# Optimization experiments

Hardware: AMD Instinct MI355X
Metric: run time of the kernel (lower is better)

## Reference

```python
import jax, jax.numpy as jnp
import numpy as np


def setup_inputs() -> dict:
    key = jax.random.key(0)
    k1, k2, k3, k4, k5 = jax.random.split(key, 5)
    n_nodes, input_dim, hidden1 = 100000, 512, 128
    z_dim = hidden1 // 2
    n_edges = 1000000
    X = jax.random.normal(k1, (n_nodes, input_dim), dtype=jnp.float32)
    W = jax.random.normal(k2, (input_dim, hidden1), dtype=jnp.float32) * 0.05
    W2 = jax.random.normal(k3, (hidden1, z_dim), dtype=jnp.float32) * 0.05
    train_edges = jax.random.randint(k4, (n_edges, 2), 0, n_nodes, dtype=jnp.int64)
    train_false_edges = jax.random.randint(k5, (n_edges, 2), 0, n_nodes, dtype=jnp.int64)
    return {"X": X, "W": W, "W2": W2,
            "train_edges": train_edges, "train_false_edges": train_false_edges}


def _decode(z, edges):
    # fused gather -> elementwise mult -> row sum over all edges at once
    # z: [N, d], edges: [E, 2] -> [E, 1]
    return jnp.sum(z[edges[:, 0]] * z[edges[:, 1]], axis=-1, keepdims=True)


def reference(X, W, W2, train_edges, train_false_edges):
    # encode: note torch.mm(adj, x) in the original is dead code; output is
    # activation(x @ W), so adj never affects the result.
    h = jax.nn.relu(X @ W)          # [N, hidden1]
    z = h @ W2                      # [N, z_dim] (identity activation)
    z1 = _decode(z, train_edges)        # [E, 1]
    z2 = _decode(z, train_false_edges)  # [E, 1]
    return jax.nn.sigmoid(jnp.concatenate([z1, z2], axis=0))  # [2E, 1]
```

## Files before the change

### kernel.cpp

```cpp
#include <hip/hip_runtime.h>
#include <hip/hip_bf16.h>
#include <hip/hip_fp16.h>
#include <math.h>

#define IN_DIM 512
#define H1     128
#define ZD     64

typedef __attribute__((ext_vector_type(8))) short bf16x8;
typedef __attribute__((ext_vector_type(4))) float f32x4;

__device__ __forceinline__ ushort f32_to_bf16_bits(float x) {
    unsigned b = __float_as_uint(x);
    unsigned r = (b + 0x7FFF + ((b >> 16) & 1)) >> 16;
    return (ushort)r;
}

__global__ void prepack_w(const float* __restrict__ W,
                          ushort* __restrict__ Whi, ushort* __restrict__ Wlo) {
    int t = blockIdx.x * 256 + threadIdx.x;
    int s  = t >> 9;
    int cb = (t >> 6) & 7;
    int l  = t & 63;
    ushort h[8], lo[8];
    #pragma unroll
    for (int j = 0; j < 8; ++j) {
        int k   = s * 32 + ((l >> 4) * 8) + j;
        int col = cb * 16 + (l & 15);
        float x = W[(size_t)k * H1 + col];
        ushort hb = f32_to_bf16_bits(x);
        float  hf = __uint_as_float((unsigned)hb << 16);
        h[j]  = hb;
        lo[j] = f32_to_bf16_bits(x - hf);
    }
    size_t off = ((size_t)t) * 8;
    *(ushort4*)&Whi[off]     = make_ushort4(h[0], h[1], h[2], h[3]);
    *(ushort4*)&Whi[off + 4] = make_ushort4(h[4], h[5], h[6], h[7]);
    *(ushort4*)&Wlo[off]     = make_ushort4(lo[0], lo[1], lo[2], lo[3]);
    *(ushort4*)&Wlo[off + 4] = make_ushort4(lo[4], lo[5], lo[6], lo[7]);
}

__global__ __launch_bounds__(256, 4) void encode_kernel(
    const float* __restrict__ X, const ushort* __restrict__ Whi,
    const ushort* __restrict__ Wlo, const float* __restrict__ W2,
    __half* __restrict__ Z, int N)
{
    __shared__ __align__(16) union {
        ushort st[2][2][4][512];
        float  ht[H1][68];
    } sm;

    const int tid  = threadIdx.x;
    const int lane = tid & 63;
    const int w    = tid >> 6;
    const int wr   = w >> 1;
    const int wc   = w & 1;
    const int row0 = blockIdx.x * 64;

    const int srow = tid >> 2;
    const int kq   = tid & 3;
    const int srb  = srow >> 4;
    const int sla  = (srow & 15) | (kq << 4);
    const bool srow_ok = (row0 + srow) < N;
    const float* xp = X + (size_t)(row0 + srow) * IN_DIM + kq * 8;

    f32x4 acc[2][4];
    #pragma unroll
    for (int i = 0; i < 2; ++i)
        #pragma unroll
        for (int j = 0; j < 4; ++j) acc[i][j] = (f32x4){0.f, 0.f, 0.f, 0.f};

    float4 rgA, rgB;
    rgA = srow_ok ? *(const float4*)(xp + 0) : make_float4(0, 0, 0, 0);
    rgB = srow_ok ? *(const float4*)(xp + 4) : make_float4(0, 0, 0, 0);

    auto stage = [&](int buf) {
        float xv[8] = {rgA.x, rgA.y, rgA.z, rgA.w, rgB.x, rgB.y, rgB.z, rgB.w};
        unsigned hb[8], lb[8];
        #pragma unroll
        for (int j = 0; j < 8; ++j) {
            unsigned b = __float_as_uint(xv[j]);
            unsigned hf = b & 0xFFFF0000u;
            hb[j] = b;
            lb[j] = __float_as_uint(xv[j] - __uint_as_float(hf));
        }
        uint4 hp, lp;
        hp.x = (hb[0] >> 16) | (hb[1] & 0xFFFF0000u);
        hp.y = (hb[2] >> 16) | (hb[3] & 0xFFFF0000u);
        hp.z = (hb[4] >> 16) | (hb[5] & 0xFFFF0000u);
        hp.w = (hb[6] >> 16) | (hb[7] & 0xFFFF0000u);
        lp.x = (lb[0] >> 16) | (lb[1] & 0xFFFF0000u);
        lp.y = (lb[2] >> 16) | (lb[3] & 0xFFFF0000u);
        lp.z = (lb[4] >> 16) | (lb[5] & 0xFFFF0000u);
        lp.w = (lb[6] >> 16) | (lb[7] & 0xFFFF0000u);
        *(uint4*)&sm.st[buf][0][srb][sla * 8] = hp;
        *(uint4*)&sm.st[buf][1][srb][sla * 8] = lp;
    };

    stage(0);
    rgA = srow_ok ? *(const float4*)(xp + 32) : make_float4(0, 0, 0, 0);
    rgB = srow_ok ? *(const float4*)(xp + 36) : make_float4(0, 0, 0, 0);
    __syncthreads();

    for (int s = 0; s < 16; ++s) {
        const int buf = s & 1;
        bf16x8 aH[2], aL[2];
        #pragma unroll
        for (int rb = 0; rb < 2; ++rb) {
            int rbg = wr * 2 + rb;
            aH[rb] = *(const bf16x8*)&sm.st[buf][0][rbg][lane * 8];
            aL[rb] = *(const bf16x8*)&sm.st[buf][1][rbg][lane * 8];
        }
        if (s < 15) stage(buf ^ 1);
        if (s < 14) {
            const float* xp2 = xp + (s + 2) * 32;
            rgA = srow_ok ? *(const float4*)(xp2 + 0) : make_float4(0, 0, 0, 0);
            rgB = srow_ok ? *(const float4*)(xp2 + 4) : make_float4(0, 0, 0, 0);
        }
        #pragma unroll
        for (int cb = 0; cb < 4; ++cb) {
            int cbg = wc * 4 + cb;
            size_t off = ((size_t)(s * 8 + cbg) * 64 + lane) * 8;
            bf16x8 bH = *(const bf16x8*)&Whi[off];
            bf16x8 bL = *(const bf16x8*)&Wlo[off];
            #pragma unroll
            for (int rb = 0; rb < 2; ++rb) {
                acc[rb][cb] = __builtin_amdgcn_mfma_f32_16x16x32_bf16(
                    aH[rb], bH, acc[rb][cb], 0, 0, 0);
                acc[rb][cb] = __builtin_amdgcn_mfma_f32_16x16x32_bf16(
                    aH[rb], bL, acc[rb][cb], 0, 0, 0);
                acc[rb][cb] = __builtin_amdgcn_mfma_f32_16x16x32_bf16(
                    aL[rb], bH, acc[rb][cb], 0, 0, 0);
            }
        }
        __syncthreads();
    }

    #pragma unroll
    for (int rb = 0; rb < 2; ++rb)
        #pragma unroll
        for (int cb = 0; cb < 4; ++cb) {
            int col = wc * 64 + cb * 16 + (lane & 15);
            int rr  = wr * 32 + rb * 16 + (lane >> 4) * 4;
            #pragma unroll
            for (int r = 0; r < 4; ++r)
                sm.ht[col][rr + r] = fmaxf(acc[rb][cb][r], 0.f);
        }
    __syncthreads();

    const int tx = tid & 31;
    const int ty = tid >> 5;

    float zacc[8][2];
    #pragma unroll
    for (int i = 0; i < 8; ++i) { zacc[i][0] = 0.f; zacc[i][1] = 0.f; }

    #pragma unroll 4
    for (int k = 0; k < H1; ++k) {
        float2 b  = *(const float2*)&W2[(size_t)k * ZD + tx * 2];
        float4 h0 = *(const float4*)&sm.ht[k][ty * 8];
        float4 h1 = *(const float4*)&sm.ht[k][ty * 8 + 4];
        float a[8] = {h0.x, h0.y, h0.z, h0.w, h1.x, h1.y, h1.z, h1.w};
        #pragma unroll
        for (int i = 0; i < 8; ++i) {
            zacc[i][0] = fmaf(a[i], b.x, zacc[i][0]);
            zacc[i][1] = fmaf(a[i], b.y, zacc[i][1]);
        }
    }
    #pragma unroll
    for (int i = 0; i < 8; ++i) {
        int gr = row0 + ty * 8 + i;
        if (gr < N)
            *(__half2*)&Z[(size_t)gr * ZD + tx * 2] =
                __floats2half2_rn(zacc[i][0], zacc[i][1]);
    }
}

__global__ __launch_bounds__(256) void decode_kernel(
    const __half* __restrict__ Zh, const int* __restrict__ e1,
    const int* __restrict__ e2, float* __restrict__ out, int E)
{
    const int tid  = threadIdx.x;
    const int lane = tid & 63;
    const int wv   = tid >> 6;
    const int sub  = lane >> 3;
    const int l    = lane & 7;
    const int total = 2 * E;
    const int stride = gridDim.x * 32;

    for (int idx = (blockIdx.x * 4 + wv) * 8 + sub; idx < total; idx += stride) {
        const int* ep = (idx < E) ? (e1 + 2 * (size_t)idx)
                                  : (e2 + 2 * (size_t)(idx - E));
        int2 ab = *(const int2*)ep;
        union { uint4 u; __half2 h[4]; } A, B;
        A.u = *(const uint4*)&Zh[(size_t)ab.x * ZD + l * 8];
        B.u = *(const uint4*)&Zh[(size_t)ab.y * ZD + l * 8];
        float s = 0.f;
        #pragma unroll
        for (int j = 0; j < 4; ++j) {
            float2 fa = __half22float2(A.h[j]);
            float2 fb = __half22float2(B.h[j]);
            s += fa.x * fb.x + fa.y * fb.y;
        }
        s += __shfl_xor(s, 4, 64);
        s += __shfl_xor(s, 2, 64);
        s += __shfl_xor(s, 1, 64);
        if (l == 0) out[idx] = 1.f / (1.f + __expf(-s));
    }
}

extern "C" void kernel_launch(void* const* d_in, const int* in_sizes, int n_in,
                              void* d_out, int out_size, void* d_ws, size_t ws_size,
                              hipStream_t stream) {
    const float* X  = (const float*)d_in[0];
    const float* W  = (const float*)d_in[1];
    const float* W2 = (const float*)d_in[2];
    const int*   e1 = (const int*)d_in[3];
    const int*   e2 = (const int*)d_in[4];
    float* out = (float*)d_out;

    const int N = in_sizes[0] / IN_DIM;
    const int E = in_sizes[3] / 2;

    __half* Zh  = (__half*)d_ws;
    ushort* Whi = (ushort*)((char*)d_ws + 12800000);
    ushort* Wlo = (ushort*)((char*)d_ws + 12800000 + 131072);

    prepack_w<<<32, 256, 0, stream>>>(W, Whi, Wlo);

    const int nblk = (N + 63) / 64;
    encode_kernel<<<nblk, 256, 0, stream>>>(X, Whi, Wlo, W2, Zh, N);

    decode_kernel<<<2048, 256, 0, stream>>>(Zh, e1, e2, out, E);
}
```

Baseline: 398.0 us.

## Bucket edges by node range before decode and shrink encode hidden staging to fp16

Adds a scatter pass that groups all edges into 128 buckets keyed by the source and destination node ranges. A new decode kernel then walks each bucket, so the Z row gathers from one block hit a narrower address range and should reuse cache better. This costs an extra pass that writes and re-reads 16-byte records, and edges beyond a fixed per-bucket capacity are silently dropped, which is only safe for roughly uniform indices. The encode kernel also stores the ReLU hidden tile as fp16 rather than fp32, raises the launch-bounds occupancy target, and remaps the X staging threads, at some cost in precision.

```diff
diff --git a/kernel.cpp b/kernel.cpp
--- a/kernel.cpp
+++ b/kernel.cpp
@@ -6,6 +6,9 @@
 #define IN_DIM 512
 #define H1     128
 #define ZD     64
+
+#define NBKT   128
+#define BCAP   18432
 
 typedef __attribute__((ext_vector_type(8))) short bf16x8;
 typedef __attribute__((ext_vector_type(4))) float f32x4;
@@ -40,14 +43,14 @@
     *(ushort4*)&Wlo[off + 4] = make_ushort4(lo[4], lo[5], lo[6], lo[7]);
 }
 
-__global__ __launch_bounds__(256, 4) void encode_kernel(
+__global__ __launch_bounds__(256, 8) void encode_kernel(
     const float* __restrict__ X, const ushort* __restrict__ Whi,
     const ushort* __restrict__ Wlo, const float* __restrict__ W2,
     __half* __restrict__ Z, int N)
 {
     __shared__ __align__(16) union {
         ushort st[2][2][4][512];
-        float  ht[H1][68];
+        __half ht[H1][72];
     } sm;
 
     const int tid  = threadIdx.x;
@@ -57,10 +60,10 @@
     const int wc   = w & 1;
     const int row0 = blockIdx.x * 64;
 
-    const int srow = tid >> 2;
-    const int kq   = tid & 3;
-    const int srb  = srow >> 4;
-    const int sla  = (srow & 15) | (kq << 4);
+    const int srb  = tid >> 6;
+    const int sla  = tid & 63;
+    const int srow = srb * 16 + (tid & 15);
+    const int kq   = (tid >> 4) & 3;
     const bool srow_ok = (row0 + srow) < N;
     const float* xp = X + (size_t)(row0 + srow) * IN_DIM + kq * 8;
 
@@ -142,9 +145,10 @@
         for (int cb = 0; cb < 4; ++cb) {
             int col = wc * 64 + cb * 16 + (lane & 15);
             int rr  = wr * 32 + rb * 16 + (lane >> 4) * 4;
-            #pragma unroll
-            for (int r = 0; r < 4; ++r)
-                sm.ht[col][rr + r] = fmaxf(acc[rb][cb][r], 0.f);
+            *(__half2*)&sm.ht[col][rr] =
+                __floats2half2_rn(fmaxf(acc[rb][cb][0], 0.f), fmaxf(acc[rb][cb][1], 0.f));
+            *(__half2*)&sm.ht[col][rr + 2] =
+                __floats2half2_rn(fmaxf(acc[rb][cb][2], 0.f), fmaxf(acc[rb][cb][3], 0.f));
         }
     __syncthreads();
 
@@ -157,14 +161,16 @@
 
     #pragma unroll 4
     for (int k = 0; k < H1; ++k) {
-        float2 b  = *(const float2*)&W2[(size_t)k * ZD + tx * 2];
-        float4 h0 = *(const float4*)&sm.ht[k][ty * 8];
-        float4 h1 = *(const float4*)&sm.ht[k][ty * 8 + 4];
-        float a[8] = {h0.x, h0.y, h0.z, h0.w, h1.x, h1.y, h1.z, h1.w};
-        #pragma unroll
-        for (int i = 0; i < 8; ++i) {
-            zacc[i][0] = fmaf(a[i], b.x, zacc[i][0]);
-            zacc[i][1] = fmaf(a[i], b.y, zacc[i][1]);
+        float2 b = *(const float2*)&W2[(size_t)k * ZD + tx * 2];
+        union { uint4 u; __half2 h[4]; } hv;
+        hv.u = *(const uint4*)&sm.ht[k][ty * 8];
+        #pragma unroll
+        for (int q = 0; q < 4; ++q) {
+            float2 fa = __half22float2(hv.h[q]);
+            zacc[2 * q][0]     = fmaf(fa.x, b.x, zacc[2 * q][0]);
+            zacc[2 * q][1]     = fmaf(fa.x, b.y, zacc[2 * q][1]);
+            zacc[2 * q + 1][0] = fmaf(fa.y, b.x, zacc[2 * q + 1][0]);
+            zacc[2 * q + 1][1] = fmaf(fa.y, b.y, zacc[2 * q + 1][1]);
         }
     }
     #pragma unroll
@@ -173,6 +179,87 @@
         if (gr < N)
             *(__half2*)&Z[(size_t)gr * ZD + tx * 2] =
                 __floats2half2_rn(zacc[i][0], zacc[i][1]);
+    }
+}
+
+__global__ void init_cursors(int* __restrict__ cursors) {
+    int t = threadIdx.x;
+    if (t < NBKT) cursors[t] = t * BCAP;
+}
+
+__global__ __launch_bounds__(256) void scatter_kernel(
+    const int* __restrict__ e1, const int* __restrict__ e2,
+    int4* __restrict__ recs, int* __restrict__ cursors, int E, float invA, float invB)
+{
+    __shared__ int lhist[NBKT];
+    __shared__ int lcur[NBKT];
+    const int tid = threadIdx.x;
+    const int total = 2 * E;
+    const int chunk = (total + gridDim.x - 1) / gridDim.x;
+    const int start = blockIdx.x * chunk;
+    const int end   = min(start + chunk, total);
+
+    for (int i = tid; i < NBKT; i += 256) lhist[i] = 0;
+    __syncthreads();
+
+    for (int i = start + tid; i < end; i += 256) {
+        int2 ab = (i < E) ? *(const int2*)&e1[2 * (size_t)i]
+                          : *(const int2*)&e2[2 * (size_t)(i - E)];
+        int as = min((int)(ab.x * invA), 7);
+        int bs = min((int)(ab.y * invB), 15);
+        atomicAdd(&lhist[as * 16 + bs], 1);
+    }
+    __syncthreads();
+    for (int i = tid; i < NBKT; i += 256)
+        lcur[i] = atomicAdd(&cursors[i], lhist[i]);
+    __syncthreads();
+
+    for (int i = start + tid; i < end; i += 256) {
+        int2 ab = (i < E) ? *(const int2*)&e1[2 * (size_t)i]
+                          : *(const int2*)&e2[2 * (size_t)(i - E)];
+        int as = min((int)(ab.x * invA), 7);
+        int bs = min((int)(ab.y * invB), 15);
+        int bkt = as * 16 + bs;
+        int pos = atomicAdd(&lcur[bkt], 1);
+        if (pos < (bkt + 1) * BCAP)
+            recs[pos] = make_int4(ab.x, ab.y, i, 0);
+    }
+}
+
+__global__ __launch_bounds__(256) void decode_sorted(
+    const __half* __restrict__ Zh, const int4* __restrict__ recs,
+    const int* __restrict__ cursors, float* __restrict__ out)
+{
+    const int k = blockIdx.x & 7;
+    const int m = blockIdx.x >> 3;
+    const int j = m >> 4;
+    const int t = m & 15;
+    const int p = k * 16 + j;
+    const int start = p * BCAP;
+    const int end   = min(cursors[p], start + BCAP);
+
+    const int tid  = threadIdx.x;
+    const int lane = tid & 63;
+    const int wv   = tid >> 6;
+    const int sub  = lane >> 3;
+    const int l    = lane & 7;
+
+    for (int r = start + t * 32 + wv * 8 + sub; r < end; r += 512) {
+        int4 rec = recs[r];
+        union { uint4 u; __half2 h[4]; } A, B;
+        A.u = *(const uint4*)&Zh[(size_t)rec.x * ZD + l * 8];
+        B.u = *(const uint4*)&Zh[(size_t)rec.y * ZD + l * 8];
+        float s = 0.f;
+        #pragma unroll
+        for (int q = 0; q < 4; ++q) {
+            float2 fa = __half22float2(A.h[q]);
+            float2 fb = __half22float2(B.h[q]);
+            s += fa.x * fb.x + fa.y * fb.y;
+        }
+        s += __shfl_xor(s, 4, 64);
+        s += __shfl_xor(s, 2, 64);
+        s += __shfl_xor(s, 1, 64);
+        if (l == 0) out[rec.z] = 1.f / (1.f + __expf(-s));
     }
 }
 
@@ -197,9 +284,9 @@
         B.u = *(const uint4*)&Zh[(size_t)ab.y * ZD + l * 8];
         float s = 0.f;
         #pragma unroll
-        for (int j = 0; j < 4; ++j) {
-            float2 fa = __half22float2(A.h[j]);
-            float2 fb = __half22float2(B.h[j]);
+        for (int q = 0; q < 4; ++q) {
+            float2 fa = __half22float2(A.h[q]);
+            float2 fb = __half22float2(B.h[q]);
             s += fa.x * fb.x + fa.y * fb.y;
         }
         s += __shfl_xor(s, 4, 64);
@@ -222,14 +309,31 @@
     const int N = in_sizes[0] / IN_DIM;
     const int E = in_sizes[3] / 2;
 
-    __half* Zh  = (__half*)d_ws;
-    ushort* Whi = (ushort*)((char*)d_ws + 12800000);
-    ushort* Wlo = (ushort*)((char*)d_ws + 12800000 + 131072);
+    const size_t ZH_OFF  = 0;
+    const size_t WHI_OFF = 12800000;
+    const size_t WLO_OFF = WHI_OFF + 131072;
+    const size_t CUR_OFF = WLO_OFF + 131072;
+    const size_t REC_OFF = CUR_OFF + 512;
+    const size_t NEEDED  = REC_OFF + (size_t)NBKT * BCAP * 16;
+
+    __half* Zh  = (__half*)((char*)d_ws + ZH_OFF);
+    ushort* Whi = (ushort*)((char*)d_ws + WHI_OFF);
+    ushort* Wlo = (ushort*)((char*)d_ws + WLO_OFF);
+    int*    cur = (int*)((char*)d_ws + CUR_OFF);
+    int4*   rec = (int4*)((char*)d_ws + REC_OFF);
 
     prepack_w<<<32, 256, 0, stream>>>(W, Whi, Wlo);
 
     const int nblk = (N + 63) / 64;
     encode_kernel<<<nblk, 256, 0, stream>>>(X, Whi, Wlo, W2, Zh, N);
 
-    decode_kernel<<<2048, 256, 0, stream>>>(Zh, e1, e2, out, E);
-}
+    if (ws_size >= NEEDED) {
+        init_cursors<<<1, 128, 0, stream>>>(cur);
+        float invA = 8.0f / (float)N;
+        float invB = 16.0f / (float)N;
+        scatter_kernel<<<256, 256, 0, stream>>>(e1, e2, rec, cur, E, invA, invB);
+        decode_sorted<<<2048, 256, 0, stream>>>(Zh, rec, cur, out);
+    } else {
+        decode_kernel<<<2048, 256, 0, stream>>>(Zh, e1, e2, out, E);
+    }
+}
```

New measurement: 637.2 us. 1.6x slower.
